# Performance work log

Hardware: AMD Instinct MI355X
Metric: run time of the kernel (lower is better)

The kernel has to match this reference:

```python
import jax, jax.numpy as jnp
import numpy as np

B, IN, H = 4096, 1024, 2048


def setup_inputs() -> dict:
    key = jax.random.key(0)
    k1, k2, k3, k4 = jax.random.split(key, 4)
    x = jax.random.normal(k1, (B, IN), dtype=jnp.float32)
    h_prev = jax.random.normal(k2, (B, H), dtype=jnp.float32)
    c_prev = jax.random.normal(k3, (B, H), dtype=jnp.float32)
    # Fused weight for the 5 gate Linears (Wf, Wi, Wc, Wo, We), columns stacked.
    # Scaled like PyTorch Linear default init (~uniform(-1/sqrt(fan_in))).
    W = jax.random.normal(k4, (IN + H, 5 * H), dtype=jnp.float32) / jnp.sqrt(jnp.float32(IN + H))
    b = jnp.zeros((5 * H,), dtype=jnp.float32)
    return {"x": x, "h_prev": h_prev, "c_prev": c_prev, "W": W, "b": b}


def reference(x, h_prev, c_prev, W, b):
    combined = jnp.concatenate([x, h_prev], axis=1)          # [B, IN+H]
    z = combined @ W + b                                      # [B, 5H] single fused GEMM
    f, i, c_hat, o, e = jnp.split(z, 5, axis=1)
    ft = jax.nn.sigmoid(f)
    it = jax.nn.sigmoid(i)
    ct_hat = jnp.tanh(c_hat)
    ot = jax.nn.sigmoid(o)
    et = jax.nn.sigmoid(e)
    ct = ft * c_prev + it * ct_hat
    ht = ot * jnp.tanh(ct)
    ht = et * jnp.exp(ht) + (1.0 - et) * ht
    return ht, ct
```

## Files before the change

### kernel.cpp

```cpp
#include <hip/hip_runtime.h>
#include <hip/hip_bf16.h>
#include <stdint.h>

#define B_  4096
#define IN_ 1024
#define H_  2048
#define K_  (IN_ + H_)
#define N_  (5 * H_)

#define BM 128
#define BJ 32
#define BK 32

typedef __attribute__((ext_vector_type(8))) short   short8;
typedef __attribute__((ext_vector_type(4))) float   f32x4;
typedef __attribute__((ext_vector_type(8))) unsigned short ushort8;

__device__ __forceinline__ unsigned short f2bf(float f) {
  union { float f; unsigned u; } cv; cv.f = f;
  unsigned u = cv.u;
  u += 0x7fffu + ((u >> 16) & 1u);
  return (unsigned short)(u >> 16);
}

__device__ __forceinline__ void async16(const unsigned short* g, unsigned short* l) {
  __builtin_amdgcn_global_load_lds(
      (const __attribute__((address_space(1))) unsigned int*)g,
      (__attribute__((address_space(3))) unsigned int*)(void*)l,
      16, 0, 0);
}

__device__ __forceinline__ float fsig(float x) {
  return __builtin_amdgcn_rcpf(1.f + __expf(-x));
}
__device__ __forceinline__ float ftanh(float x) {
  return 1.f - 2.f * __builtin_amdgcn_rcpf(__expf(2.f * x) + 1.f);
}

__global__ void build_combined(const float* __restrict__ x,
                               const float* __restrict__ h,
                               unsigned short* __restrict__ out) {
  const int row = blockIdx.x;
  const float4* xr = (const float4*)(x + (size_t)row * IN_);
  const float4* hr = (const float4*)(h + (size_t)row * H_);
  uint2* orow = (uint2*)(out + (size_t)row * K_);
  for (int c = threadIdx.x; c < K_ / 4; c += 256) {
    float4 v = (c < IN_ / 4) ? xr[c] : hr[c - IN_ / 4];
    uint2 p;
    p.x = (unsigned)f2bf(v.x) | ((unsigned)f2bf(v.y) << 16);
    p.y = (unsigned)f2bf(v.z) | ((unsigned)f2bf(v.w) << 16);
    orow[c] = p;
  }
}

__global__ __launch_bounds__(256) void transpose_convert(
    const float* __restrict__ W, unsigned short* __restrict__ Wt) {
  __shared__ float tile[64][65];
  const int n0 = blockIdx.x * 64;
  const int k0 = blockIdx.y * 64;
  const int t  = threadIdx.x;

  const int r0 = t >> 4;
  const int c4 = t & 15;
  #pragma unroll
  for (int i = 0; i < 4; ++i) {
    const int kk = i * 16 + r0;
    const float4 v = *(const float4*)&W[(size_t)(k0 + kk) * N_ + n0 + c4 * 4];
    float* dst = &tile[kk][c4 * 4];
    dst[0] = v.x; dst[1] = v.y; dst[2] = v.z; dst[3] = v.w;
  }
  __syncthreads();

  #pragma unroll
  for (int i = 0; i < 2; ++i) {
    const int c2 = t + i * 256;
    const int nn = c2 >> 3;
    const int kc = (c2 & 7) * 8;
    ushort8 p;
    #pragma unroll
    for (int u = 0; u < 8; ++u) p[u] = f2bf(tile[kc + u][nn]);
    *(ushort8*)&Wt[(size_t)(n0 + nn) * K_ + k0 + kc] = p;
  }
}

__global__ __launch_bounds__(256, 3) void gemm_fused(
    const unsigned short* __restrict__ A,
    const unsigned short* __restrict__ Bt,
    const float* __restrict__ c_prev,
    const float* __restrict__ bias,
    float* __restrict__ out)
{
  __shared__ unsigned short As[BM * BK];
  __shared__ unsigned short Bs[5 * BJ * BK];

  const int tid  = threadIdx.x;
  const int wave = tid >> 6;
  const int lane = tid & 63;
  const int quad = lane >> 4;
  const int lr   = lane & 15;

  const int tile_m = blockIdx.x >> 6;
  const int tile_j = blockIdx.x & 63;
  const int m0 = tile_m * BM;
  const int j0 = tile_j * BJ;

  const int wm = (wave & 1) * 64;
  const int wn = (wave >> 1) * 16;

  f32x4 acc[4][5];
  #pragma unroll
  for (int mi = 0; mi < 4; ++mi)
    #pragma unroll
    for (int g = 0; g < 5; ++g)
      acc[mi][g] = (f32x4){0.f, 0.f, 0.f, 0.f};

  const int lrow4 = lane >> 2;
  const int scol  = ((lane & 3) ^ ((lane >> 3) & 3)) * 8;
  const size_t k16 = (size_t)16 * K_;

  const unsigned short* aP =
      A + ((size_t)(m0 + wave * 32 + lrow4)) * K_ + scol;
  unsigned short* aL0 = &As[(wave * 32) * BK];
  unsigned short* aL1 = &As[(wave * 32 + 16) * BK];

  const unsigned short* bBase = Bt + ((size_t)(j0 + lrow4)) * K_ + scol;
  const unsigned short* bP0 = bBase + (size_t)wave * H_ * K_;
  const unsigned short* bP2 = bBase + ((size_t)4 * H_ + wave * 16) * K_;
  unsigned short* bL0 = &Bs[(wave * 32) * BK];
  unsigned short* bL1 = &Bs[(wave * 32 + 16) * BK];
  unsigned short* bL2 = &Bs[((8 + wave) * 16) * BK];
  const bool doTail = (wave < 2);

  const int rslot = (quad ^ ((lr >> 1) & 3)) * 8;

  for (int k0 = 0; k0 < K_; k0 += BK) {
    async16(aP + k0,        aL0);
    async16(aP + k16 + k0,  aL1);
    async16(bP0 + k0,       bL0);
    async16(bP0 + k16 + k0, bL1);
    if (doTail) async16(bP2 + k0, bL2);
    __syncthreads();

    short8 af[4], bf[5];
    #pragma unroll
    for (int mi = 0; mi < 4; ++mi)
      af[mi] = *(const short8*)&As[(wm + mi * 16 + lr) * BK + rslot];
    #pragma unroll
    for (int g = 0; g < 5; ++g)
      bf[g] = *(const short8*)&Bs[(g * 32 + wn + lr) * BK + rslot];

    #pragma unroll
    for (int mi = 0; mi < 4; ++mi)
      #pragma unroll
      for (int g = 0; g < 5; ++g)
        acc[mi][g] = __builtin_amdgcn_mfma_f32_16x16x32_bf16(
            af[mi], bf[g], acc[mi][g], 0, 0, 0);

    __syncthreads();
  }

  const int col = j0 + wn + lr;
  float bb[5];
  #pragma unroll
  for (int g = 0; g < 5; ++g) bb[g] = bias[g * H_ + col];

  #pragma unroll
  for (int mi = 0; mi < 4; ++mi) {
    const int rbase = m0 + wm + mi * 16 + quad * 4;
    float cp[4];
    #pragma unroll
    for (int r = 0; r < 4; ++r)
      cp[r] = c_prev[(size_t)(rbase + r) * H_ + col];
    #pragma unroll
    for (int r = 0; r < 4; ++r) {
      const float ft = fsig(acc[mi][0][r] + bb[0]);
      const float it = fsig(acc[mi][1][r] + bb[1]);
      const float ch = ftanh(acc[mi][2][r] + bb[2]);
      const float ot = fsig(acc[mi][3][r] + bb[3]);
      const float et = fsig(acc[mi][4][r] + bb[4]);
      const float ct = ft * cp[r] + it * ch;
      const float th = ftanh(ct);
      float ht = ot * th;
      ht = et * __expf(ht) + (1.f - et) * ht;
      out[(size_t)(rbase + r) * H_ + col] = ht;
      out[(size_t)B_ * H_ + (size_t)(rbase + r) * H_ + col] = ct;
    }
  }
}

extern "C" void kernel_launch(void* const* d_in, const int* in_sizes, int n_in,
                              void* d_out, int out_size, void* d_ws, size_t ws_size,
                              hipStream_t stream) {
  const float* x = (const float*)d_in[0];
  const float* h = (const float*)d_in[1];
  const float* c = (const float*)d_in[2];
  const float* W = (const float*)d_in[3];
  const float* b = (const float*)d_in[4];
  float* out = (float*)d_out;

  char* ws = (char*)d_ws;
  unsigned short* combined = (unsigned short*)ws;
  unsigned short* Wt = (unsigned short*)(ws + (size_t)25165824);

  build_combined<<<B_, 256, 0, stream>>>(x, h, combined);
  transpose_convert<<<dim3(N_ / 64, K_ / 64), 256, 0, stream>>>(W, Wt);
  gemm_fused<<<(B_ / BM) * (H_ / BJ), 256, 0, stream>>>(combined, Wt, c, b, out);
}
```

Before: 529.6 us.

## Double-buffer GEMM LDS tiles with async prefetch two stages ahead

Turns the single-buffered LDS tiles in the fused LSTM GEMM into two buffers, with the global-to-LDS async loads issued two K-steps ahead. Explicit vmcnt/lgkmcnt waits and raw s_barrier replace the two __syncthreads per iteration, so global loads overlap with MFMA work. The MFMA block also gets a raised wave priority. The cost is double the LDS (about 28KB per block), which may limit occupancy, and fragile hand-counted waitcnt values.

```diff
diff --git a/kernel.cpp b/kernel.cpp
--- a/kernel.cpp
+++ b/kernel.cpp
@@ -11,6 +11,7 @@
 #define BM 128
 #define BJ 32
 #define BK 32
+#define NT 96
 
 typedef __attribute__((ext_vector_type(8))) short   short8;
 typedef __attribute__((ext_vector_type(4))) float   f32x4;
@@ -90,8 +91,8 @@
     const float* __restrict__ bias,
     float* __restrict__ out)
 {
-  __shared__ unsigned short As[BM * BK];
-  __shared__ unsigned short Bs[5 * BJ * BK];
+  __shared__ unsigned short As[2][BM * BK];
+  __shared__ unsigned short Bs[2][5 * BJ * BK];
 
   const int tid  = threadIdx.x;
   const int wave = tid >> 6;
@@ -120,44 +121,65 @@
 
   const unsigned short* aP =
       A + ((size_t)(m0 + wave * 32 + lrow4)) * K_ + scol;
-  unsigned short* aL0 = &As[(wave * 32) * BK];
-  unsigned short* aL1 = &As[(wave * 32 + 16) * BK];
+  const int aL0o = (wave * 32) * BK;
+  const int aL1o = (wave * 32 + 16) * BK;
 
   const unsigned short* bBase = Bt + ((size_t)(j0 + lrow4)) * K_ + scol;
   const unsigned short* bP0 = bBase + (size_t)wave * H_ * K_;
   const unsigned short* bP2 = bBase + ((size_t)4 * H_ + wave * 16) * K_;
-  unsigned short* bL0 = &Bs[(wave * 32) * BK];
-  unsigned short* bL1 = &Bs[(wave * 32 + 16) * BK];
-  unsigned short* bL2 = &Bs[((8 + wave) * 16) * BK];
+  const int bL0o = (wave * 32) * BK;
+  const int bL1o = (wave * 32 + 16) * BK;
+  const int bL2o = ((8 + wave) * 16) * BK;
   const bool doTail = (wave < 2);
 
+  #define STAGE(tt, bb) do {                          \
+    const int ko_ = (tt) * BK;                        \
+    async16(aP + ko_,        &As[(bb)][aL0o]);        \
+    async16(aP + k16 + ko_,  &As[(bb)][aL1o]);        \
+    async16(bP0 + ko_,       &Bs[(bb)][bL0o]);        \
+    async16(bP0 + k16 + ko_, &Bs[(bb)][bL1o]);        \
+    if (doTail) async16(bP2 + ko_, &Bs[(bb)][bL2o]);  \
+  } while (0)
+
+  STAGE(0, 0);
+  STAGE(1, 1);
+
   const int rslot = (quad ^ ((lr >> 1) & 3)) * 8;
 
-  for (int k0 = 0; k0 < K_; k0 += BK) {
-    async16(aP + k0,        aL0);
-    async16(aP + k16 + k0,  aL1);
-    async16(bP0 + k0,       bL0);
-    async16(bP0 + k16 + k0, bL1);
-    if (doTail) async16(bP2 + k0, bL2);
-    __syncthreads();
+  #pragma unroll 2
+  for (int t = 0; t < NT; ++t) {
+    const int cur = t & 1;
+
+    if (t == NT - 1)     asm volatile("s_waitcnt vmcnt(0)" ::: "memory");
+    else if (doTail)     asm volatile("s_waitcnt vmcnt(5)" ::: "memory");
+    else                 asm volatile("s_waitcnt vmcnt(4)" ::: "memory");
+    __builtin_amdgcn_s_barrier();
 
     short8 af[4], bf[5];
     #pragma unroll
     for (int mi = 0; mi < 4; ++mi)
-      af[mi] = *(const short8*)&As[(wm + mi * 16 + lr) * BK + rslot];
+      af[mi] = *(const short8*)&As[cur][(wm + mi * 16 + lr) * BK + rslot];
     #pragma unroll
     for (int g = 0; g < 5; ++g)
-      bf[g] = *(const short8*)&Bs[(g * 32 + wn + lr) * BK + rslot];
-
+      bf[g] = *(const short8*)&Bs[cur][(g * 32 + wn + lr) * BK + rslot];
+
+    asm volatile("s_waitcnt lgkmcnt(0)" ::: "memory");
+    __builtin_amdgcn_sched_barrier(0);
+    __builtin_amdgcn_s_barrier();
+
+    if (t < NT - 2) STAGE(t + 2, cur);
+    __builtin_amdgcn_sched_barrier(0);
+
+    __builtin_amdgcn_s_setprio(1);
     #pragma unroll
     for (int mi = 0; mi < 4; ++mi)
       #pragma unroll
       for (int g = 0; g < 5; ++g)
         acc[mi][g] = __builtin_amdgcn_mfma_f32_16x16x32_bf16(
             af[mi], bf[g], acc[mi][g], 0, 0, 0);
-
-    __syncthreads();
-  }
+    __builtin_amdgcn_s_setprio(0);
+  }
+  #undef STAGE
 
   const int col = j0 + wn + lr;
   float bb[5];
```

Result: no change. 526.2 us (-0.6%).
